# Optimization experiments

Hardware: AMD Instinct MI355X
Metric: run time of the kernel (lower is better)

The kernel has to match this reference:

```python
import jax, jax.numpy as jnp
import numpy as np

D = 8        # input_path_dim (number of driving channels / base vector fields)
N = 256      # cde_state_dim
H = 512      # vf_hidden_dim
B = 4096     # batch of evaluation points (vmapped calls)
P = D * (D - 1) // 2            # number of depth-2 Lyndon brackets (i<j)
M = D + P                       # total brackets = depth-2 Lyndon basis size
_II, _JJ = np.triu_indices(D, k=1)   # Lyndon words (i,j), i<j


def _mlp_fields(h, W1, b1, W2, b2, W3, b3, Wo, bo):
    # eqx.nn.MLP(in=N, out=D*N, width=H, depth=3, softplus hidden, tanh final)
    x = jax.nn.softplus(W1 @ h + b1)
    x = jax.nn.softplus(W2 @ x + b2)
    x = jax.nn.softplus(W3 @ x + b3)
    return jnp.tanh(Wo @ x + bo).reshape(D, N)   # V_i(h), i=1..D


def setup_inputs() -> dict:
    key = jax.random.key(0)
    ks = jax.random.split(key, 10)

    def lin(kw, kb, out_dim, in_dim):
        lim = 1.0 / np.sqrt(in_dim)
        W = jax.random.uniform(kw, (out_dim, in_dim), minval=-lim, maxval=lim, dtype=jnp.float32)
        b = jax.random.uniform(kb, (out_dim,), minval=-lim, maxval=lim, dtype=jnp.float32)
        return W, b

    W1, b1 = lin(ks[0], ks[1], H, N)
    W2, b2 = lin(ks[2], ks[3], H, H)
    W3, b3 = lin(ks[4], ks[5], H, H)
    Wo, bo = lin(ks[6], ks[7], D * N, H)
    h = jax.random.normal(ks[8], (B, N), dtype=jnp.float32)
    primitive_signature = jax.random.normal(ks[9], (B, M), dtype=jnp.float32) * 0.1
    return {
        "h": h, "primitive_signature": primitive_signature,
        "W1": W1, "b1": b1, "W2": W2, "b2": b2,
        "W3": W3, "b3": b3, "Wo": Wo, "bo": bo,
    }


def reference(h, primitive_signature, W1, b1, W2, b2, W3, b3, Wo, bo):
    def single(hv, sig):
        F = lambda y: _mlp_fields(y, W1, b1, W2, b2, W3, b3, Wo, bo)  # [D, N]
        V = F(hv)                                                      # level-1 brackets V_i(h)
        # J[k, i] = DV_i(h) @ V_k(h); one jvp per base-field direction
        J = jax.vmap(lambda v: jax.jvp(F, (hv,), (v,))[1])(V)          # [D, D, N]
        # Lyndon lift, depth 2: [V_i, V_j](h) = DV_j V_i - DV_i V_j, i<j
        lvl2 = J[_II, _JJ] - J[_JJ, _II]                               # [P, N]
        brackets = jnp.concatenate([V, lvl2], axis=0)                  # [M, N]
        # log-ODE contraction against primitive log-signature coefficients
        return jnp.einsum("mn,m->n", brackets, sig)                    # [N]

    return jax.vmap(single)(h, primitive_signature)                    # [B, N]
```

## Files before the change

kernel.cpp:

```cpp
#include <hip/hip_runtime.h>
#include <hip/hip_bf16.h>
#include <math.h>

#define MM 36

typedef _Float16 f16;
typedef __attribute__((ext_vector_type(8))) _Float16 f16x8;
typedef __attribute__((ext_vector_type(4))) _Float16 f16x4;
typedef __attribute__((ext_vector_type(4))) float f32x4;

enum { EPI_NONE = 0, EPI_SP = 1, EPI_TANH = 2, EPI_GATE = 3 };

__device__ __forceinline__ void gl_lds16(const f16* g, f16* l) {
    __builtin_amdgcn_global_load_lds(
        (const __attribute__((address_space(1))) void*)g,
        (__attribute__((address_space(3))) void*)l, 16, 0, 0);
}

__global__ __launch_bounds__(512, 2) void gemm8p(
    const f16* __restrict__ A, int lda,
    const f16* __restrict__ W, int ldw,
    f16* __restrict__ C, int ldc,
    const f16* __restrict__ G,
    int K)
{
    __shared__ __align__(16) f16 smem[49152];
    f16* bufA = smem;
    f16* bufB = smem + 24576;

    const int t = threadIdx.x;
    const int nxy = gridDim.x * gridDim.y;
    const int orig = blockIdx.x + gridDim.x * blockIdx.y;
    const int q = nxy >> 3, r = nxy & 7;
    const int xcd = orig & 7, idx = orig >> 3;
    const int nid = (xcd < r ? xcd * (q + 1) : r * (q + 1) + (xcd - r) * q) + idx;
    const long rowTile = (long)(nid >> 1) * 256;
    const long colTile = (long)(nid & 1) * 256;

    const int wave = t >> 6;
    const int lane = t & 63;
    const int wm = wave >> 2;
    const int wn = wave & 3;
    const int lr = lane & 15;
    const int lk = lane >> 4;
    const int rq = lk ^ (lr & 3);

    const int srow = t >> 2;
    const int skq  = t & 3;

    f32x4 acc[8][4];
    const f32x4 zero = {0.f, 0.f, 0.f, 0.f};
#pragma unroll
    for (int m = 0; m < 8; ++m)
#pragma unroll
        for (int n = 0; n < 4; ++n) acc[m][n] = zero;

    const int nt = K >> 5;

    auto stageA = [&](int buf, int tk) {
        const int k0 = tk << 5;
#pragma unroll
        for (int p = 0; p < 2; ++p) {
            const int row = srow + p * 128;
            gl_lds16(A + (rowTile + row) * (long)lda + k0 + (skq ^ (row & 3)) * 8,
                     &bufA[buf * 8192 + (p * 512 + t) * 8]);
        }
    };
    auto stageB = [&](int buf, int tk) {
        const int k0 = tk << 5;
#pragma unroll
        for (int p = 0; p < 2; ++p) {
            const int row = srow + p * 128;
            gl_lds16(W + (colTile + row) * (long)ldw + k0 + (skq ^ (row & 3)) * 8,
                     &bufB[buf * 8192 + (p * 512 + t) * 8]);
        }
    };

    stageA(0, 0); stageB(0, 0);
    stageA(1, 1); stageB(1, 1);
    asm volatile("s_waitcnt vmcnt(4)" ::: "memory");
    __builtin_amdgcn_s_barrier();

    for (int tk = 0; tk < nt; ++tk) {
        const int cb = tk % 3;
        const int sb = (tk + 2) % 3;
        const f16* At = &bufA[cb * 8192];
        const f16* Bt = &bufB[cb * 8192];
        f16x8 a[4], b[4];
#pragma unroll
        for (int m = 0; m < 4; ++m)
            a[m] = *(const f16x8*)&At[(wm * 128 + m * 16 + lr) * 32 + rq * 8];
#pragma unroll
        for (int n = 0; n < 4; ++n)
            b[n] = *(const f16x8*)&Bt[(wn * 64 + n * 16 + lr) * 32 + rq * 8];
        if (tk + 2 < nt) stageA(sb, tk + 2);
        __builtin_amdgcn_s_setprio(1);
#pragma unroll
        for (int m = 0; m < 4; ++m)
#pragma unroll
            for (int n = 0; n < 4; ++n)
                acc[m][n] = __builtin_amdgcn_mfma_f32_16x16x32_f16(a[m], b[n], acc[m][n], 0, 0, 0);
        __builtin_amdgcn_s_setprio(0);
#pragma unroll
        for (int m = 0; m < 4; ++m)
            a[m] = *(const f16x8*)&At[(wm * 128 + (m + 4) * 16 + lr) * 32 + rq * 8];
        if (tk + 2 < nt) stageB(sb, tk + 2);
        __builtin_amdgcn_s_setprio(1);
#pragma unroll
        for (int m = 0; m < 4; ++m)
#pragma unroll
            for (int n = 0; n < 4; ++n)
                acc[m + 4][n] = __builtin_amdgcn_mfma_f32_16x16x32_f16(a[m], b[n], acc[m + 4][n], 0, 0, 0);
        __builtin_amdgcn_s_setprio(0);
        if (tk + 1 < nt) {
            if (tk + 2 < nt) asm volatile("s_waitcnt vmcnt(4)" ::: "memory");
            else             asm volatile("s_waitcnt vmcnt(0)" ::: "memory");
            __builtin_amdgcn_s_barrier();
        }
    }

#pragma unroll
    for (int half = 0; half < 2; ++half) {
        __builtin_amdgcn_s_barrier();
        if (wm == half) {
#pragma unroll
            for (int m = 0; m < 8; ++m)
#pragma unroll
                for (int n = 0; n < 4; ++n)
#pragma unroll
                    for (int j = 0; j < 4; ++j) {
                        const int lrow = m * 16 + lk * 4 + j;
                        const int lcol = wn * 64 + n * 16 + lr;
                        const long row = rowTile + half * 128 + lrow;
                        const float s = (float)G[(row >> 3) * ldc + colTile + lcol];
                        const float g = 1.f - __expf(-s);
                        smem[lrow * 256 + (lcol ^ (lk * 16))] = (f16)(acc[m][n][j] * g);
                    }
        }
        __builtin_amdgcn_s_barrier();
#pragma unroll
        for (int p = 0; p < 8; ++p) {
            const int c = p * 512 + t;
            const int rl = c >> 5;
            const int c16 = (c & 31) * 8;
            const f16x8 v = *(const f16x8*)&smem[rl * 256 + (c16 ^ (((rl >> 2) & 3) * 16))];
            *(f16x8*)&C[(rowTile + half * 128 + rl) * ldc + colTile + c16] = v;
        }
    }
}

template <int EPI, int BM, int BN, int TPB, int WN>
__global__ __launch_bounds__(TPB, 4) void gemm16(
    const f16* __restrict__ A, int lda, long aZ,
    const f16* __restrict__ W, int ldw, long wZ,
    const float* __restrict__ bias,
    void* __restrict__ C0v, int ldc, long cZ,
    const f16* __restrict__ G,
    int K, int cshift)
{
    constexpr int WM = TPB / 64 / WN;
    constexpr int FM = BM / (WM * 16);
    constexpr int FN = BN / (WN * 16);
    constexpr int LA = BM * 4 / TPB;
    constexpr int LB = BN * 4 / TPB;

    __shared__ __align__(16) f16 smem[2 * (BM + BN) * 32];
    f16* As0 = smem;
    f16* Ws0 = smem + 2 * BM * 32;

    const int t = threadIdx.x;
    const int z = blockIdx.z;
    A += (size_t)z * aZ;
    W += (size_t)z * wZ;

    const int nxy = gridDim.x * gridDim.y;
    const int orig = blockIdx.x + gridDim.x * blockIdx.y;
    const int q = nxy >> 3, r = nxy & 7;
    const int xcd = orig & 7, idx = orig >> 3;
    const int nid = (xcd < r ? xcd * (q + 1) : r * (q + 1) + (xcd - r) * q) + idx;
    const long rowTile = (long)(nid >> cshift) * BM;
    const long colTile = (long)(nid & ((1 << cshift) - 1)) * BN;

    const int wave = t >> 6;
    const int lane = t & 63;
    const int wr = (wave / WN) * (FM * 16);
    const int wc = (wave % WN) * (FN * 16);
    const int lr = lane & 15;
    const int lk = lane >> 4;

    const f16* Ag = A + (rowTile + (t >> 2)) * lda + (t & 3) * 8;
    const f16* Wg = W + (colTile + (t >> 2)) * ldw + (t & 3) * 8;

    f32x4 acc[FM][FN];
    const f32x4 zero = {0.f, 0.f, 0.f, 0.f};
#pragma unroll
    for (int m = 0; m < FM; ++m)
#pragma unroll
        for (int n = 0; n < FN; ++n) acc[m][n] = zero;

    const int nt = K >> 5;

    auto stage = [&](int buf, int k0) {
#pragma unroll
        for (int p = 0; p < LA; ++p)
            gl_lds16(Ag + (long)p * (TPB / 4) * lda + k0, &As0[buf * (BM * 32) + (p * TPB + t) * 8]);
#pragma unroll
        for (int p = 0; p < LB; ++p)
            gl_lds16(Wg + (long)p * (TPB / 4) * ldw + k0, &Ws0[buf * (BN * 32) + (p * TPB + t) * 8]);
    };

    stage(0, 0);

    for (int ti = 0; ti < nt; ++ti) {
        const int buf = ti & 1;
        __syncthreads();
        if (ti + 1 < nt) stage(buf ^ 1, (ti + 1) << 5);
        f16x8 a[FM], b[FN];
#pragma unroll
        for (int m = 0; m < FM; ++m)
            a[m] = *(const f16x8*)&As0[buf * (BM * 32) + (wr + m * 16 + lr) * 32 + lk * 8];
#pragma unroll
        for (int n = 0; n < FN; ++n)
            b[n] = *(const f16x8*)&Ws0[buf * (BN * 32) + (wc + n * 16 + lr) * 32 + lk * 8];
#pragma unroll
        for (int m = 0; m < FM; ++m)
#pragma unroll
            for (int n = 0; n < FN; ++n)
                acc[m][n] = __builtin_amdgcn_mfma_f32_16x16x32_f16(a[m], b[n], acc[m][n], 0, 0, 0);
    }

    const int erow = t >> 4;
    const int ecq  = (t & 15) * 8;

    __syncthreads();
#pragma unroll
    for (int m = 0; m < FM; ++m) {
#pragma unroll
        for (int n = 0; n < FN; ++n) {
            const int lcol = wc + n * 16 + lr;
            const float bb = bias ? bias[colTile + lcol] : 0.f;
#pragma unroll
            for (int j = 0; j < 4; ++j) {
                const int lrow = wr + m * 16 + lk * 4 + j;
                const int lidx = lrow * BN + (lcol ^ (lk * 16));
                const float x = acc[m][n][j] + bb;
                if constexpr (EPI == EPI_SP) {
                    const float e = __expf(-fabsf(x));
                    smem[lidx] = (f16)(fmaxf(x, 0.f) + __logf(1.f + e));
                } else if constexpr (EPI == EPI_TANH) {
                    const float e2 = __expf(2.f * x);
                    smem[lidx] = (f16)(1.f - 2.f * __builtin_amdgcn_rcpf(e2 + 1.f));
                } else if constexpr (EPI == EPI_GATE) {
                    const long row = rowTile + lrow;
                    const float s = (float)G[(row >> 3) * ldc + colTile + lcol];
                    smem[lidx] = (f16)(x * (1.f - __expf(-s)));
                } else {
                    smem[lidx] = (f16)x;
                }
            }
        }
    }
    __syncthreads();
    {
        f16* dst = (EPI == EPI_NONE) ? ((f16*)C0v + (size_t)z * cZ) : (f16*)C0v;
#pragma unroll
        for (int p = 0; p < BM / 16; ++p) {
            const int row = p * 16 + erow;
            const f16x8 v = *(const f16x8*)&smem[row * BN + (ecq ^ (((row >> 2) & 3) * 16))];
            *(f16x8*)&dst[(rowTile + row) * ldc + colTile + ecq] = v;
        }
    }
}

__global__ __launch_bounds__(256) void ktilde16(
    const f16* __restrict__ V, const float* __restrict__ sig,
    f16* __restrict__ T, int b0)
{
    const int bl = blockIdx.x * 4 + (threadIdx.x >> 6);
    const int n0 = (threadIdx.x & 63) * 4;
    const f16* vb = V + (size_t)bl * 2048 + n0;
    float v[8][4];
#pragma unroll
    for (int k = 0; k < 8; ++k) {
        const f16x4 x = *(const f16x4*)&vb[k * 256];
#pragma unroll
        for (int j = 0; j < 4; ++j) v[k][j] = (float)x[j];
    }
    const float* sg = sig + (size_t)(b0 + bl) * MM + 8;
    float s2[28];
#pragma unroll
    for (int p = 0; p < 28; ++p) s2[p] = sg[p];

    f16* tb = T + (size_t)bl * 2048 + n0;
#pragma unroll
    for (int i = 0; i < 8; ++i) {
        float a0 = 0.f, a1 = 0.f, a2 = 0.f, a3 = 0.f;
#pragma unroll
        for (int k = 0; k < 8; ++k) {
            if (k == i) continue;
            const int a = (k < i) ? k : i;
            const int b = (k < i) ? i : k;
            const int p = a * (15 - a) / 2 + (b - a - 1);
            const float c = (k < i) ? s2[p] : -s2[p];
            a0 = fmaf(c, v[k][0], a0); a1 = fmaf(c, v[k][1], a1);
            a2 = fmaf(c, v[k][2], a2); a3 = fmaf(c, v[k][3], a3);
        }
        f16x4 o;
        o[0] = (f16)a0; o[1] = (f16)a1; o[2] = (f16)a2; o[3] = (f16)a3;
        *(f16x4*)&tb[i * 256] = o;
    }
}

__global__ __launch_bounds__(256) void finish16(
    const f16* __restrict__ V, const f16* __restrict__ Oi,
    const float* __restrict__ sig, float* __restrict__ out, int b0, int C)
{
    const int bl = blockIdx.x * 4 + (threadIdx.x >> 6);
    const int n0 = (threadIdx.x & 63) * 4;
    const float* sg = sig + (size_t)(b0 + bl) * MM;
    float a0 = 0.f, a1 = 0.f, a2 = 0.f, a3 = 0.f;
#pragma unroll
    for (int i = 0; i < 8; ++i) {
        const f16x4 vv = *(const f16x4*)&V[(size_t)bl * 2048 + i * 256 + n0];
        const f16x4 oo = *(const f16x4*)&Oi[((size_t)i * C + bl) * 256 + n0];
        const float s = sg[i];
        const float v0 = (float)vv[0], v1 = (float)vv[1];
        const float v2 = (float)vv[2], v3 = (float)vv[3];
        a0 = fmaf(s, v0, a0); a0 = fmaf(1.f - v0 * v0, (float)oo[0], a0);
        a1 = fmaf(s, v1, a1); a1 = fmaf(1.f - v1 * v1, (float)oo[1], a1);
        a2 = fmaf(s, v2, a2); a2 = fmaf(1.f - v2 * v2, (float)oo[2], a2);
        a3 = fmaf(s, v3, a3); a3 = fmaf(1.f - v3 * v3, (float)oo[3], a3);
    }
    float4 ov; ov.x = a0; ov.y = a1; ov.z = a2; ov.w = a3;
    *(float4*)&out[(size_t)(b0 + bl) * 256 + n0] = ov;
}

__global__ __launch_bounds__(256) void cvtW(
    const float* __restrict__ W1, const float* __restrict__ W2,
    const float* __restrict__ W3, const float* __restrict__ Wo,
    f16* __restrict__ o1, f16* __restrict__ o2,
    f16* __restrict__ o3, f16* __restrict__ oo)
{
    long i = (long)blockIdx.x * 256 + threadIdx.x;
    const float* src; f16* dst; long base;
    if (i < 32768)       { src = W1; dst = o1; base = 0; }
    else if (i < 98304)  { src = W2; dst = o2; base = 32768; }
    else if (i < 163840) { src = W3; dst = o3; base = 98304; }
    else                 { src = Wo; dst = oo; base = 163840; }
    i -= base;
    const float4 v = ((const float4*)src)[i];
    f16x4 o;
    o[0] = (f16)v.x; o[1] = (f16)v.y; o[2] = (f16)v.z; o[3] = (f16)v.w;
    ((f16x4*)dst)[i] = o;
}

__global__ __launch_bounds__(256) void cvt16(
    const float* __restrict__ x, f16* __restrict__ y, int n)
{
    const int i = (blockIdx.x * 256 + threadIdx.x) * 4;
    if (i < n) {
        const float4 v = *(const float4*)&x[i];
        f16x4 o;
        o[0] = (f16)v.x; o[1] = (f16)v.y; o[2] = (f16)v.z; o[3] = (f16)v.w;
        *(f16x4*)&y[i] = o;
    }
}

extern "C" void kernel_launch(void* const* d_in, const int* in_sizes, int n_in,
                              void* d_out, int out_size, void* d_ws, size_t ws_size,
                              hipStream_t stream) {
    const float* h   = (const float*)d_in[0];
    const float* sig = (const float*)d_in[1];
    const float* W1  = (const float*)d_in[2];
    const float* b1  = (const float*)d_in[3];
    const float* W2  = (const float*)d_in[4];
    const float* b2  = (const float*)d_in[5];
    const float* W3  = (const float*)d_in[6];
    const float* b3  = (const float*)d_in[7];
    const float* Wo  = (const float*)d_in[8];
    const float* bo  = (const float*)d_in[9];
    float* out = (float*)d_out;

    char* p = (char*)d_ws;
    f16* W1h = (f16*)p; p += (size_t)512 * 256 * 2;
    f16* W2h = (f16*)p; p += (size_t)512 * 512 * 2;
    f16* W3h = (f16*)p; p += (size_t)512 * 512 * 2;
    f16* Woh = (f16*)p; p += (size_t)2048 * 512 * 2;
    const size_t fixed = (size_t)(p - (char*)d_ws);

    int C = 4096;
    while (C > 128 && fixed + (size_t)C * 28160 > ws_size) C >>= 1;

    f16* h16 = (f16*)p; p += (size_t)C * 256 * 2;
    f16* s1 = (f16*)p;  p += (size_t)C * 512 * 2;
    f16* s2 = (f16*)p;  p += (size_t)C * 512 * 2;
    f16* s3 = (f16*)p;  p += (size_t)C * 512 * 2;
    f16* V  = (f16*)p;  p += (size_t)C * 2048 * 2;
    f16* T  = (f16*)p;  p += (size_t)C * 2048 * 2;
    f16* Ua = (f16*)p;  p += (size_t)C * 4096 * 2;
    f16* Ub = (f16*)p;
    f16* Oi = Ub;

    const dim3 blk(256);
    const dim3 blk8(512);
    cvtW<<<dim3(1664), blk, 0, stream>>>(W1, W2, W3, Wo, W1h, W2h, W3h, Woh);

    for (int b0 = 0; b0 < 4096; b0 += C) {
        cvt16<<<dim3(C * 256 / 1024), blk, 0, stream>>>(h + (size_t)b0 * 256, h16, C * 256);
        gemm16<EPI_SP, 64, 128, 256, 4><<<dim3(4, C / 64), blk, 0, stream>>>(
            h16, 256, 0, W1h, 256, 0, b1, s1, 512, 0, nullptr, 256, 2);
        gemm16<EPI_SP, 64, 128, 256, 4><<<dim3(4, C / 64), blk, 0, stream>>>(
            s1, 512, 0, W2h, 512, 0, b2, s2, 512, 0, nullptr, 512, 2);
        gemm16<EPI_SP, 64, 128, 256, 4><<<dim3(4, C / 64), blk, 0, stream>>>(
            s2, 512, 0, W3h, 512, 0, b3, s3, 512, 0, nullptr, 512, 2);
        gemm16<EPI_TANH, 128, 128, 256, 2><<<dim3(16, C / 128), blk, 0, stream>>>(
            s3, 512, 0, Woh, 512, 0, bo, V, 2048, 0, nullptr, 512, 4);
        ktilde16<<<dim3(C / 4), blk, 0, stream>>>(V, sig, T, b0);
        gemm8p<<<dim3(2, C * 8 / 256), blk8, 0, stream>>>(
            T, 256, W1h, 256, Ua, 512, s1, 256);
        gemm8p<<<dim3(2, C * 8 / 256), blk8, 0, stream>>>(
            Ua, 512, W2h, 512, Ub, 512, s2, 512);
        gemm8p<<<dim3(2, C * 8 / 256), blk8, 0, stream>>>(
            Ub, 512, W3h, 512, Ua, 512, s3, 512);
        gemm16<EPI_NONE, 128, 128, 256, 2><<<dim3(2, C / 128, 8), blk, 0, stream>>>(
            Ua, 4096, 512, Woh, 512, (long)256 * 512, nullptr, Oi, 256, (long)C * 256,
            nullptr, 512, 1);
        finish16<<<dim3(C / 4), blk, 0, stream>>>(V, Oi, sig, out, b0, C);
    }
}
```

Before: 163.5 us.

## Triple-buffer gemm16 LDS pipeline with XOR-swizzled loads and fewer barriers

Replaces the double-buffered gemm16 main loop with a three-stage LDS pipeline that keeps two tiles of global loads in flight. Explicit vmcnt waits plus a single raw barrier per k-step replace the __syncthreads-before-stage pattern. The 16-byte k-chunks are XOR-swizzled by row to cut LDS bank conflicts on the fragment reads, and s_setprio is raised around the MFMA block. The extra LDS buffer lowers the occupancy bound to 3 for the larger tiles, and the unused gate epilogue is dropped.

```diff
diff --git a/kernel.cpp b/kernel.cpp
--- a/kernel.cpp
+++ b/kernel.cpp
@@ -150,12 +150,11 @@
 }
 
 template <int EPI, int BM, int BN, int TPB, int WN>
-__global__ __launch_bounds__(TPB, 4) void gemm16(
+__global__ __launch_bounds__(TPB, ((BM + BN) <= 192) ? 4 : 3) void gemmCV(
     const f16* __restrict__ A, int lda, long aZ,
     const f16* __restrict__ W, int ldw, long wZ,
     const float* __restrict__ bias,
-    void* __restrict__ C0v, int ldc, long cZ,
-    const f16* __restrict__ G,
+    f16* __restrict__ C, int ldc, long cZ,
     int K, int cshift)
 {
     constexpr int WM = TPB / 64 / WN;
@@ -163,15 +162,17 @@
     constexpr int FN = BN / (WN * 16);
     constexpr int LA = BM * 4 / TPB;
     constexpr int LB = BN * 4 / TPB;
-
-    __shared__ __align__(16) f16 smem[2 * (BM + BN) * 32];
-    f16* As0 = smem;
-    f16* Ws0 = smem + 2 * BM * 32;
+    constexpr int L  = LA + LB;
+
+    __shared__ __align__(16) f16 smem[3 * (BM + BN) * 32];
+    f16* bufA = smem;
+    f16* bufB = smem + 3 * BM * 32;
 
     const int t = threadIdx.x;
     const int z = blockIdx.z;
     A += (size_t)z * aZ;
     W += (size_t)z * wZ;
+    C += (size_t)z * cZ;
 
     const int nxy = gridDim.x * gridDim.y;
     const int orig = blockIdx.x + gridDim.x * blockIdx.y;
@@ -187,9 +188,9 @@
     const int wc = (wave % WN) * (FN * 16);
     const int lr = lane & 15;
     const int lk = lane >> 4;
-
-    const f16* Ag = A + (rowTile + (t >> 2)) * lda + (t & 3) * 8;
-    const f16* Wg = W + (colTile + (t >> 2)) * ldw + (t & 3) * 8;
+    const int rq = lk ^ (lr & 3);
+    const int srow = t >> 2;
+    const int skq  = t & 3;
 
     f32x4 acc[FM][FN];
     const f32x4 zero = {0.f, 0.f, 0.f, 0.f};
@@ -200,37 +201,57 @@
 
     const int nt = K >> 5;
 
-    auto stage = [&](int buf, int k0) {
-#pragma unroll
-        for (int p = 0; p < LA; ++p)
-            gl_lds16(Ag + (long)p * (TPB / 4) * lda + k0, &As0[buf * (BM * 32) + (p * TPB + t) * 8]);
-#pragma unroll
-        for (int p = 0; p < LB; ++p)
-            gl_lds16(Wg + (long)p * (TPB / 4) * ldw + k0, &Ws0[buf * (BN * 32) + (p * TPB + t) * 8]);
+    auto stage = [&](int buf, int tk) {
+        const int k0 = tk << 5;
+#pragma unroll
+        for (int p = 0; p < LA; ++p) {
+            const int row = srow + p * (TPB / 4);
+            gl_lds16(A + (rowTile + row) * (long)lda + k0 + (skq ^ (row & 3)) * 8,
+                     &bufA[buf * (BM * 32) + (p * TPB + t) * 8]);
+        }
+#pragma unroll
+        for (int p = 0; p < LB; ++p) {
+            const int row = srow + p * (TPB / 4);
+            gl_lds16(W + (colTile + row) * (long)ldw + k0 + (skq ^ (row & 3)) * 8,
+                     &bufB[buf * (BN * 32) + (p * TPB + t) * 8]);
+        }
     };
+    auto waitL = [&]() {
+        if constexpr (L == 3) asm volatile("s_waitcnt vmcnt(3)" ::: "memory");
+        else if constexpr (L == 4) asm volatile("s_waitcnt vmcnt(4)" ::: "memory");
+        else asm volatile("s_waitcnt vmcnt(0)" ::: "memory");
+    };
 
     stage(0, 0);
-
-    for (int ti = 0; ti < nt; ++ti) {
-        const int buf = ti & 1;
-        __syncthreads();
-        if (ti + 1 < nt) stage(buf ^ 1, (ti + 1) << 5);
+    stage(1, 1);
+    waitL();
+    __builtin_amdgcn_s_barrier();
+
+    for (int tk = 0; tk < nt; ++tk) {
+        const int cb = tk % 3;
+        const f16* At = &bufA[cb * (BM * 32)];
+        const f16* Bt = &bufB[cb * (BN * 32)];
         f16x8 a[FM], b[FN];
 #pragma unroll
         for (int m = 0; m < FM; ++m)
-            a[m] = *(const f16x8*)&As0[buf * (BM * 32) + (wr + m * 16 + lr) * 32 + lk * 8];
+            a[m] = *(const f16x8*)&At[(wr + m * 16 + lr) * 32 + rq * 8];
 #pragma unroll
         for (int n = 0; n < FN; ++n)
-            b[n] = *(const f16x8*)&Ws0[buf * (BN * 32) + (wc + n * 16 + lr) * 32 + lk * 8];
+            b[n] = *(const f16x8*)&Bt[(wc + n * 16 + lr) * 32 + rq * 8];
+        if (tk + 2 < nt) stage((tk + 2) % 3, tk + 2);
+        __builtin_amdgcn_s_setprio(1);
 #pragma unroll
         for (int m = 0; m < FM; ++m)
 #pragma unroll
             for (int n = 0; n < FN; ++n)
                 acc[m][n] = __builtin_amdgcn_mfma_f32_16x16x32_f16(a[m], b[n], acc[m][n], 0, 0, 0);
-    }
-
-    const int erow = t >> 4;
-    const int ecq  = (t & 15) * 8;
+        __builtin_amdgcn_s_setprio(0);
+        if (tk + 1 < nt) {
+            if (tk + 2 < nt) waitL();
+            else asm volatile("s_waitcnt vmcnt(0)" ::: "memory");
+            __builtin_amdgcn_s_barrier();
+        }
+    }
 
     __syncthreads();
 #pragma unroll
@@ -250,10 +271,6 @@
                 } else if constexpr (EPI == EPI_TANH) {
                     const float e2 = __expf(2.f * x);
                     smem[lidx] = (f16)(1.f - 2.f * __builtin_amdgcn_rcpf(e2 + 1.f));
-                } else if constexpr (EPI == EPI_GATE) {
-                    const long row = rowTile + lrow;
-                    const float s = (float)G[(row >> 3) * ldc + colTile + lcol];
-                    smem[lidx] = (f16)(x * (1.f - __expf(-s)));
                 } else {
                     smem[lidx] = (f16)x;
                 }
@@ -261,14 +278,13 @@
         }
     }
     __syncthreads();
-    {
-        f16* dst = (EPI == EPI_NONE) ? ((f16*)C0v + (size_t)z * cZ) : (f16*)C0v;
-#pragma unroll
-        for (int p = 0; p < BM / 16; ++p) {
-            const int row = p * 16 + erow;
-            const f16x8 v = *(const f16x8*)&smem[row * BN + (ecq ^ (((row >> 2) & 3) * 16))];
-            *(f16x8*)&dst[(rowTile + row) * ldc + colTile + ecq] = v;
-        }
+#pragma unroll
+    for (int p = 0; p < BM * BN / (8 * TPB); ++p) {
+        const int c = p * TPB + t;
+        const int rl = c / (BN / 8);
+        const int c16 = (c % (BN / 8)) * 8;
+        const f16x8 v = *(const f16x8*)&smem[rl * BN + (c16 ^ (((rl >> 2) & 3) * 16))];
+        *(f16x8*)&C[(rowTile + rl) * ldc + colTile + c16] = v;
     }
 }
 
@@ -407,14 +423,14 @@
 
     for (int b0 = 0; b0 < 4096; b0 += C) {
         cvt16<<<dim3(C * 256 / 1024), blk, 0, stream>>>(h + (size_t)b0 * 256, h16, C * 256);
-        gemm16<EPI_SP, 64, 128, 256, 4><<<dim3(4, C / 64), blk, 0, stream>>>(
-            h16, 256, 0, W1h, 256, 0, b1, s1, 512, 0, nullptr, 256, 2);
-        gemm16<EPI_SP, 64, 128, 256, 4><<<dim3(4, C / 64), blk, 0, stream>>>(
-            s1, 512, 0, W2h, 512, 0, b2, s2, 512, 0, nullptr, 512, 2);
-        gemm16<EPI_SP, 64, 128, 256, 4><<<dim3(4, C / 64), blk, 0, stream>>>(
-            s2, 512, 0, W3h, 512, 0, b3, s3, 512, 0, nullptr, 512, 2);
-        gemm16<EPI_TANH, 128, 128, 256, 2><<<dim3(16, C / 128), blk, 0, stream>>>(
-            s3, 512, 0, Woh, 512, 0, bo, V, 2048, 0, nullptr, 512, 4);
+        gemmCV<EPI_SP, 64, 128, 256, 4><<<dim3(4, C / 64), blk, 0, stream>>>(
+            h16, 256, 0, W1h, 256, 0, b1, s1, 512, 0, 256, 2);
+        gemmCV<EPI_SP, 64, 128, 256, 4><<<dim3(4, C / 64), blk, 0, stream>>>(
+            s1, 512, 0, W2h, 512, 0, b2, s2, 512, 0, 512, 2);
+        gemmCV<EPI_SP, 64, 128, 256, 4><<<dim3(4, C / 64), blk, 0, stream>>>(
+            s2, 512, 0, W3h, 512, 0, b3, s3, 512, 0, 512, 2);
+        gemmCV<EPI_TANH, 128, 128, 256, 2><<<dim3(16, C / 128), blk, 0, stream>>>(
+            s3, 512, 0, Woh, 512, 0, bo, V, 2048, 0, 512, 4);
         ktilde16<<<dim3(C / 4), blk, 0, stream>>>(V, sig, T, b0);
         gemm8p<<<dim3(2, C * 8 / 256), blk8, 0, stream>>>(
             T, 256, W1h, 256, Ua, 512, s1, 256);
@@ -422,9 +438,9 @@
             Ua, 512, W2h, 512, Ub, 512, s2, 512);
         gemm8p<<<dim3(2, C * 8 / 256), blk8, 0, stream>>>(
             Ub, 512, W3h, 512, Ua, 512, s3, 512);
-        gemm16<EPI_NONE, 128, 128, 256, 2><<<dim3(2, C / 128, 8), blk, 0, stream>>>(
+        gemmCV<EPI_NONE, 128, 128, 256, 2><<<dim3(2, C / 128, 8), blk, 0, stream>>>(
             Ua, 4096, 512, Woh, 512, (long)256 * 512, nullptr, Oi, 256, (long)C * 256,
-            nullptr, 512, 1);
+            512, 1);
         finish16<<<dim3(C / 4), blk, 0, stream>>>(V, Oi, sig, out, b0, C);
     }
 }
```

After: 160.4 us. No clear change (-1.9%).
